# Kernel tuning notes

Hardware: AMD Instinct MI355X
Metric: run time of the kernel (lower is better)

Reference implementation:

```python
import jax, jax.numpy as jnp
import numpy as np

B, S, HS = 2, 2048, 2048
H, KVH, D = 8, 1, 256
ROPE_BASE = 10000.0


def _rope_cos_sin(position_ids, dim, base=ROPE_BASE):
    # position_ids: (B, S) int -> cos/sin: (B, S, dim)
    inv_freq = 1.0 / (base ** (jnp.arange(0, dim, 2, dtype=jnp.float32) / dim))
    thetas = position_ids.astype(jnp.float32)[..., None] * inv_freq  # (B,S,dim/2)
    emb = jnp.concatenate([thetas, thetas], axis=-1)  # (B,S,dim)
    return jnp.cos(emb), jnp.sin(emb)


def _rotate_half(x):
    x1, x2 = jnp.split(x, 2, axis=-1)
    return jnp.concatenate([-x2, x1], axis=-1)


def _apply_rope(q, k, cos, sin):
    # q,k: (B,h,S,D); cos,sin: (B,S,D) -> unsqueeze head dim
    cos = cos[:, None, :, :]
    sin = sin[:, None, :, :]
    q_emb = q * cos + _rotate_half(q) * sin
    k_emb = k * cos + _rotate_half(k) * sin
    return q_emb, k_emb


def setup_inputs() -> dict:
    key = jax.random.key(0)
    k0, k1, k2, k3, k4 = jax.random.split(key, 5)
    hidden_states = jax.random.normal(k0, (B, S, HS), jnp.float32)
    # causal additive mask: 0 where j<=i, large negative otherwise
    causal = jnp.tril(jnp.ones((S, S), dtype=bool))
    attention_mask = jnp.where(causal, 0.0, -1e9).astype(jnp.float32)
    attention_mask = jnp.broadcast_to(attention_mask[None, None], (B, 1, S, S))
    position_ids = jnp.broadcast_to(jnp.arange(S, dtype=jnp.int32)[None], (B, S))
    scale = 0.02
    Wq = jax.random.normal(k1, (HS, H * D), jnp.float32) * scale
    Wk = jax.random.normal(k2, (HS, KVH * D), jnp.float32) * scale
    Wv = jax.random.normal(k3, (HS, KVH * D), jnp.float32) * scale
    Wo = jax.random.normal(k4, (H * D, HS), jnp.float32) * scale
    return {"hidden_states": hidden_states, "attention_mask": attention_mask,
            "position_ids": position_ids, "Wq": Wq, "Wk": Wk, "Wv": Wv, "Wo": Wo}


def reference(hidden_states, attention_mask, position_ids, Wq, Wk, Wv, Wo):
    bs, seq_len, _ = hidden_states.shape
    q = (hidden_states @ Wq).reshape(bs, seq_len, H, D).transpose(0, 2, 1, 3)     # (B,H,S,D)
    k = (hidden_states @ Wk).reshape(bs, seq_len, KVH, D).transpose(0, 2, 1, 3)   # (B,KVH,S,D)
    v = (hidden_states @ Wv).reshape(bs, seq_len, KVH, D).transpose(0, 2, 1, 3)
    cos, sin = _rope_cos_sin(position_ids, D)
    q, k = _apply_rope(q, k, cos, sin)
    n_rep = H // KVH
    k = jnp.repeat(k, n_rep, axis=1)  # GQA repeat -> (B,H,S,D)
    v = jnp.repeat(v, n_rep, axis=1)
    scores = jnp.einsum('bhqd,bhkd->bhqk', q, k) / jnp.sqrt(jnp.float32(D))
    scores = scores + attention_mask
    attn = jax.nn.softmax(scores.astype(jnp.float32), axis=-1).astype(q.dtype)
    out = jnp.einsum('bhqk,bhkd->bhqd', attn, v)            # (B,H,S,D)
    out = out.transpose(0, 2, 1, 3).reshape(bs, seq_len, H * D)
    return out @ Wo
```

## Files before the change

kernel.cpp:

```cpp
#include <hip/hip_runtime.h>
#include <hip/hip_bf16.h>

typedef __bf16 bf16x8 __attribute__((ext_vector_type(8)));
typedef __bf16 bf16x4 __attribute__((ext_vector_type(4)));
typedef float  f32x4  __attribute__((ext_vector_type(4)));

#define MFMA16(a, b, c) __builtin_amdgcn_mfma_f32_16x16x32_bf16((a), (b), (c), 0, 0, 0)

#define GLOBAL_AS(p) ((const __attribute__((address_space(1))) void*)(p))
#define LDS_AS(p)    ((__attribute__((address_space(3))) void*)(p))

__global__ __launch_bounds__(256) void cvt_bf16_kernel(const float* __restrict__ in,
                                                       __bf16* __restrict__ out)
{
    const int idx = blockIdx.x * 256 + threadIdx.x;
    const float4* p = (const float4*)in + (size_t)idx * 2;
    float4 a = p[0], b = p[1];
    bf16x8 o;
    o[0] = (__bf16)a.x; o[1] = (__bf16)a.y; o[2] = (__bf16)a.z; o[3] = (__bf16)a.w;
    o[4] = (__bf16)b.x; o[5] = (__bf16)b.y; o[6] = (__bf16)b.z; o[7] = (__bf16)b.w;
    ((bf16x8*)out)[idx] = o;
}

__global__ __launch_bounds__(128) void trig_kernel(float2* __restrict__ cs)
{
    const int s = blockIdx.x, i = threadIdx.x;
    const float theta = (float)s * exp2f((float)i * (-13.287712379549449f / 128.f));
    float sn, c;
    sincosf(theta, &sn, &c);
    cs[s * 128 + i] = make_float2(c, sn);
}

__global__ __launch_bounds__(256) void transpose_cvt_kernel(const float* __restrict__ W,
                                                            __bf16* __restrict__ Bt,
                                                            int K, int N)
{
    __shared__ float t[32][33];
    const int n0 = blockIdx.x * 32, k0 = blockIdx.y * 32;
    const int x = threadIdx.x, y = threadIdx.y;
#pragma unroll
    for (int r = 0; r < 4; ++r)
        t[y + r * 8][x] = W[(size_t)(k0 + y + r * 8) * N + n0 + x];
    __syncthreads();
#pragma unroll
    for (int r = 0; r < 4; ++r)
        Bt[(size_t)(n0 + y + r * 8) * K + k0 + x] = (__bf16)t[x][y + r * 8];
}

__global__ __launch_bounds__(256) void vt_kernel(const __bf16* __restrict__ qkv,
                                                 __bf16* __restrict__ vT)
{
    __shared__ __bf16 t[32][33];
    const int s0 = blockIdx.x * 32, d0 = blockIdx.y * 32, b = blockIdx.z;
    const int x = threadIdx.x, y = threadIdx.y;
#pragma unroll
    for (int r = 0; r < 4; ++r)
        t[y + r * 8][x] = qkv[(size_t)(b * 2048 + s0 + y + r * 8) * 2560 + 2304 + d0 + x];
    __syncthreads();
#pragma unroll
    for (int r = 0; r < 4; ++r)
        vT[(size_t)(b * 256 + d0 + y + r * 8) * 2048 + s0 + x] = t[x][y + r * 8];
}

template <typename TC>
__global__ __launch_bounds__(256) void gemm_bt(const __bf16* __restrict__ A,
                                               const __bf16* __restrict__ Bt,
                                               TC* __restrict__ C,
                                               int M, int N, int K)
{
    __shared__ __bf16 As[128 * 32];
    __shared__ __bf16 Bs[128 * 32];

    const int tid  = threadIdx.x;
    const int wave = tid >> 6, lane = tid & 63;
    const int quad = lane >> 4, l16 = lane & 15;
    const int wm = (wave >> 1) * 64, wn = (wave & 1) * 64;
    const int bm = blockIdx.y * 128, bn = blockIdx.x * 128;

    f32x4 acc[4][4] = {};

    for (int k0 = 0; k0 < K; k0 += 32) {
        __syncthreads();
#pragma unroll
        for (int c = 0; c < 2; ++c) {
            const int off = tid * 16 + c * 4096;
            const int row = off >> 6;
            const int kb  = (off & 63) >> 1;
            const __bf16* ga = A  + (size_t)(bm + row) * K + k0 + kb;
            const __bf16* gb = Bt + (size_t)(bn + row) * K + k0 + kb;
            __builtin_amdgcn_global_load_lds(GLOBAL_AS(ga), LDS_AS(As + (off >> 1)), 16, 0, 0);
            __builtin_amdgcn_global_load_lds(GLOBAL_AS(gb), LDS_AS(Bs + (off >> 1)), 16, 0, 0);
        }
        __syncthreads();

        bf16x8 af[4];
#pragma unroll
        for (int mi = 0; mi < 4; ++mi)
            af[mi] = *(const bf16x8*)&As[(wm + mi * 16 + l16) * 32 + quad * 8];
#pragma unroll
        for (int ni = 0; ni < 4; ++ni) {
            bf16x8 bfr = *(const bf16x8*)&Bs[(wn + ni * 16 + l16) * 32 + quad * 8];
#pragma unroll
            for (int mi = 0; mi < 4; ++mi)
                acc[mi][ni] = MFMA16(af[mi], bfr, acc[mi][ni]);
        }
    }
#pragma unroll
    for (int mi = 0; mi < 4; ++mi)
#pragma unroll
        for (int ni = 0; ni < 4; ++ni)
#pragma unroll
            for (int r = 0; r < 4; ++r) {
                int row = bm + wm + mi * 16 + quad * 4 + r;
                int col = bn + wn + ni * 16 + l16;
                C[(size_t)row * N + col] = (TC)acc[mi][ni][r];
            }
}

__global__ __launch_bounds__(256) void rope_kernel(__bf16* __restrict__ qkv,
                                                   const float2* __restrict__ cs)
{
    const int bs = blockIdx.x;
    const int s = bs & 2047;
    const int t = threadIdx.x;
    const float QS = 0.09016843787599907f;

    const int hh = t >> 5, i0 = (t & 31) * 4;
    float2 c0 = cs[s * 128 + i0 + 0], c1 = cs[s * 128 + i0 + 1];
    float2 c2 = cs[s * 128 + i0 + 2], c3 = cs[s * 128 + i0 + 3];

    {
        __bf16* p = qkv + (size_t)bs * 2560 + hh * 256 + i0;
        bf16x4 x1 = *(const bf16x4*)p;
        bf16x4 x2 = *(const bf16x4*)(p + 128);
        bf16x4 o1, o2;
        o1[0] = (__bf16)(((float)x1[0] * c0.x - (float)x2[0] * c0.y) * QS);
        o2[0] = (__bf16)(((float)x2[0] * c0.x + (float)x1[0] * c0.y) * QS);
        o1[1] = (__bf16)(((float)x1[1] * c1.x - (float)x2[1] * c1.y) * QS);
        o2[1] = (__bf16)(((float)x2[1] * c1.x + (float)x1[1] * c1.y) * QS);
        o1[2] = (__bf16)(((float)x1[2] * c2.x - (float)x2[2] * c2.y) * QS);
        o2[2] = (__bf16)(((float)x2[2] * c2.x + (float)x1[2] * c2.y) * QS);
        o1[3] = (__bf16)(((float)x1[3] * c3.x - (float)x2[3] * c3.y) * QS);
        o2[3] = (__bf16)(((float)x2[3] * c3.x + (float)x1[3] * c3.y) * QS);
        *(bf16x4*)p = o1;
        *(bf16x4*)(p + 128) = o2;
    }
    if (t < 32) {
        const int j0 = t * 4;
        float2 d0 = cs[s * 128 + j0 + 0], d1 = cs[s * 128 + j0 + 1];
        float2 d2 = cs[s * 128 + j0 + 2], d3 = cs[s * 128 + j0 + 3];
        __bf16* p = qkv + (size_t)bs * 2560 + 2048 + j0;
        bf16x4 x1 = *(const bf16x4*)p;
        bf16x4 x2 = *(const bf16x4*)(p + 128);
        bf16x4 o1, o2;
        o1[0] = (__bf16)((float)x1[0] * d0.x - (float)x2[0] * d0.y);
        o2[0] = (__bf16)((float)x2[0] * d0.x + (float)x1[0] * d0.y);
        o1[1] = (__bf16)((float)x1[1] * d1.x - (float)x2[1] * d1.y);
        o2[1] = (__bf16)((float)x2[1] * d1.x + (float)x1[1] * d1.y);
        o1[2] = (__bf16)((float)x1[2] * d2.x - (float)x2[2] * d2.y);
        o2[2] = (__bf16)((float)x2[2] * d2.x + (float)x1[2] * d2.y);
        o1[3] = (__bf16)((float)x1[3] * d3.x - (float)x2[3] * d3.y);
        o2[3] = (__bf16)((float)x2[3] * d3.x + (float)x1[3] * d3.y);
        *(bf16x4*)p = o1;
        *(bf16x4*)(p + 128) = o2;
    }
}

static __device__ __forceinline__ void stage8(const __bf16* src, __bf16* dst,
                                              size_t src_step)
{
#pragma unroll
    for (int p = 0; p < 8; ++p)
        __builtin_amdgcn_global_load_lds(GLOBAL_AS(src + (size_t)p * src_step),
                                         LDS_AS(dst + p * 2048), 16, 0, 0);
}

__global__ __launch_bounds__(256, 2) void attn_kernel(const __bf16* __restrict__ qkv,
                                                      const __bf16* __restrict__ vTg,
                                                      __bf16* __restrict__ og)
{
    __shared__ __bf16 Ks[64 * 256];
    __shared__ __bf16 Vs[256 * 64];
    __shared__ __bf16 Ps[4][32][36];

    const int b = blockIdx.z, h = blockIdx.y;
    const int xx = (int)blockIdx.x;
    const int half = xx >> 1;
    const bool rev = ((xx & 1) == 0) ^ (b != 0);
    const int qt = rev ? 31 - half : half;
    const int q0 = qt * 64;
    const int tid  = threadIdx.x;
    const int wave = tid >> 6, lane = tid & 63;
    const int quad = lane >> 4, l16 = lane & 15;
    const int xork = l16 & 7;
    const int wm2 = wave >> 1, wn2 = wave & 1;

    bf16x8 onef;
#pragma unroll
    for (int e = 0; e < 8; ++e) onef[e] = (__bf16)1.0f;

    bf16x8 qf[2][8];
#pragma unroll
    for (int mi = 0; mi < 2; ++mi) {
        const __bf16* qptr = qkv + (size_t)(b * 2048 + q0 + wm2 * 32 + mi * 16 + l16) * 2560
                           + h * 256;
#pragma unroll
        for (int dc = 0; dc < 8; ++dc)
            qf[mi][dc] = *(const bf16x8*)(qptr + dc * 32 + quad * 8);
    }

    f32x4 oacc[2][16] = {};
    f32x4 lacc[2] = {};

    const int kKey0 = tid >> 5;
    const int kC    = (tid & 31) ^ (kKey0 & 7);
    const __bf16* kstage0 = qkv + (size_t)b * 2048 * 2560 + 2048
                          + (size_t)kKey0 * 2560 + kC * 8;
    const int vD0 = tid >> 3;
    const int vC  = (tid & 7) ^ (vD0 & 7);
    const __bf16* vstage0 = vTg + (size_t)b * 256 * 2048 + (size_t)vD0 * 2048 + vC * 8;
    __bf16* kdst = Ks + tid * 8;
    __bf16* vdst = Vs + tid * 8;

    int ckK[8];
#pragma unroll
    for (int dc = 0; dc < 8; ++dc) ckK[dc] = (dc * 4 + quad) ^ xork;
    const int chV = (wn2 * 4 + quad) ^ xork;

    stage8(kstage0, kdst, (size_t)8 * 2560);
    __builtin_amdgcn_sched_barrier(0);
    stage8(vstage0, vdst, (size_t)32 * 2048);
    __builtin_amdgcn_sched_barrier(0);

    for (int j0 = 0; j0 <= q0; j0 += 64) {
        const bool more = (j0 + 64 <= q0);

        asm volatile("s_waitcnt vmcnt(8)" ::: "memory");
        __builtin_amdgcn_s_barrier();
        __builtin_amdgcn_sched_barrier(0);

        f32x4 sc[2][2] = {};
        __builtin_amdgcn_s_setprio(1);
#pragma unroll
        for (int nt = 0; nt < 2; ++nt) {
            const __bf16* krow = &Ks[(wn2 * 32 + nt * 16 + l16) * 256];
#pragma unroll
            for (int dc = 0; dc < 8; ++dc) {
                bf16x8 kf = *(const bf16x8*)(krow + ckK[dc] * 8);
                sc[0][nt] = MFMA16(qf[0][dc], kf, sc[0][nt]);
                sc[1][nt] = MFMA16(qf[1][dc], kf, sc[1][nt]);
            }
        }
        __builtin_amdgcn_s_setprio(0);

        asm volatile("s_waitcnt lgkmcnt(0)" ::: "memory");
        __builtin_amdgcn_s_barrier();
        __builtin_amdgcn_sched_barrier(0);

        if (more) {
            stage8(kstage0 + (size_t)(j0 + 64) * 2560, kdst, (size_t)8 * 2560);
            __builtin_amdgcn_sched_barrier(0);
        }

        if (j0 == q0) {
#pragma unroll
            for (int nt = 0; nt < 2; ++nt) {
                int key = j0 + wn2 * 32 + nt * 16 + l16;
#pragma unroll
                for (int mi = 0; mi < 2; ++mi)
#pragma unroll
                    for (int r = 0; r < 4; ++r) {
                        int row = q0 + wm2 * 32 + mi * 16 + quad * 4 + r;
                        if (key > row) sc[mi][nt][r] = -1e30f;
                    }
            }
        }
#pragma unroll
        for (int mi = 0; mi < 2; ++mi)
#pragma unroll
            for (int nt = 0; nt < 2; ++nt)
#pragma unroll
                for (int r = 0; r < 4; ++r)
                    Ps[wave][mi * 16 + quad * 4 + r][nt * 16 + l16] =
                        (__bf16)exp2f(sc[mi][nt][r] - 8.f);
        bf16x8 pf0 = *(const bf16x8*)&Ps[wave][l16][quad * 8];
        bf16x8 pf1 = *(const bf16x8*)&Ps[wave][16 + l16][quad * 8];

        if (more) asm volatile("s_waitcnt vmcnt(8)" ::: "memory");
        else      asm volatile("s_waitcnt vmcnt(0)" ::: "memory");
        __builtin_amdgcn_s_barrier();
        __builtin_amdgcn_sched_barrier(0);

        __builtin_amdgcn_s_setprio(1);
#pragma unroll
        for (int dt = 0; dt < 16; ++dt) {
            const __bf16* vrow = &Vs[(dt * 16 + l16) * 64];
            bf16x8 vf = *(const bf16x8*)(vrow + chV * 8);
            oacc[0][dt] = MFMA16(pf0, vf, oacc[0][dt]);
            oacc[1][dt] = MFMA16(pf1, vf, oacc[1][dt]);
        }
        lacc[0] = MFMA16(pf0, onef, lacc[0]);
        lacc[1] = MFMA16(pf1, onef, lacc[1]);
        __builtin_amdgcn_s_setprio(0);

        asm volatile("s_waitcnt lgkmcnt(0)" ::: "memory");
        __builtin_amdgcn_s_barrier();
        __builtin_amdgcn_sched_barrier(0);

        if (more) {
            stage8(vstage0 + (j0 + 64), vdst, (size_t)32 * 2048);
            __builtin_amdgcn_sched_barrier(0);
        }
    }

    __syncthreads();
    float* oscr = (wm2 == 0) ? (float*)Ks : (float*)Vs;
    float* lscr = (float*)Ps;
    if (wn2 == 1) {
#pragma unroll
        for (int mi = 0; mi < 2; ++mi) {
#pragma unroll
            for (int dt = 0; dt < 16; ++dt)
#pragma unroll
                for (int r = 0; r < 4; ++r)
                    oscr[(mi * 16 + quad * 4 + r) * 256 + dt * 16 + l16] = oacc[mi][dt][r];
#pragma unroll
            for (int r = 0; r < 4; ++r)
                lscr[(wm2 * 32 + mi * 16 + quad * 4 + r) * 16 + l16] = lacc[mi][r];
        }
    }
    __syncthreads();
    if (wn2 == 0) {
#pragma unroll
        for (int mi = 0; mi < 2; ++mi) {
            float invl[4];
#pragma unroll
            for (int r = 0; r < 4; ++r)
                invl[r] = 1.f / (lacc[mi][r]
                        + lscr[(wm2 * 32 + mi * 16 + quad * 4 + r) * 16 + l16]);
#pragma unroll
            for (int dt = 0; dt < 16; ++dt)
#pragma unroll
                for (int r = 0; r < 4; ++r) {
                    float o = oacc[mi][dt][r]
                            + oscr[(mi * 16 + quad * 4 + r) * 256 + dt * 16 + l16];
                    int row = q0 + wm2 * 32 + mi * 16 + quad * 4 + r;
                    int col = h * 256 + dt * 16 + l16;
                    og[(size_t)(b * 2048 + row) * 2048 + col] = (__bf16)(o * invl[r]);
                }
        }
    }
}

extern "C" void kernel_launch(void* const* d_in, const int* in_sizes, int n_in,
                              void* d_out, int out_size, void* d_ws, size_t ws_size,
                              hipStream_t stream)
{
    (void)in_sizes; (void)n_in; (void)out_size; (void)ws_size;
    const float* hidden = (const float*)d_in[0];
    const float* Wq = (const float*)d_in[3];
    const float* Wk = (const float*)d_in[4];
    const float* Wv = (const float*)d_in[5];
    const float* Wo = (const float*)d_in[6];

    char* ws = (char*)d_ws;
    __bf16* hb    = (__bf16*)(ws);
    __bf16* qkv   = (__bf16*)(ws + (16u << 20));
    __bf16* vTb   = (__bf16*)(ws + (36u << 20));
    __bf16* ob    = (__bf16*)(ws + (38u << 20));
    __bf16* Wqkvt = (__bf16*)(ws + (54u << 20));
    __bf16* Wot   = (__bf16*)(ws + (64u << 20));
    float2* csb   = (float2*)(ws + (72u << 20));
    float* out = (float*)d_out;

    dim3 blk(256);
    dim3 tblk(32, 8);
    cvt_bf16_kernel<<<dim3(4096), blk, 0, stream>>>(hidden, hb);
    trig_kernel<<<dim3(2048), dim3(128), 0, stream>>>(csb);
    transpose_cvt_kernel<<<dim3(64, 64), tblk, 0, stream>>>(Wq, Wqkvt, 2048, 2048);
    transpose_cvt_kernel<<<dim3(8, 64), tblk, 0, stream>>>(Wk, Wqkvt + (size_t)2048 * 2048, 2048, 256);
    transpose_cvt_kernel<<<dim3(8, 64), tblk, 0, stream>>>(Wv, Wqkvt + (size_t)2304 * 2048, 2048, 256);
    transpose_cvt_kernel<<<dim3(64, 64), tblk, 0, stream>>>(Wo, Wot, 2048, 2048);
    gemm_bt<__bf16><<<dim3(20, 32), blk, 0, stream>>>(hb, Wqkvt, qkv, 4096, 2560, 2048);
    rope_kernel<<<dim3(4096), blk, 0, stream>>>(qkv, csb);
    vt_kernel<<<dim3(64, 8, 2), tblk, 0, stream>>>(qkv, vTb);
    attn_kernel<<<dim3(32, 8, 2), blk, 0, stream>>>(qkv, vTb, ob);
    gemm_bt<float><<<dim3(16, 32), blk, 0, stream>>>(ob, Wot, out, 4096, 2048, 2048);
}
```

Measured before the change: 355.8 us.

## Replace GEMM with triple-buffered, XOR-swizzled 512-thread pipelined kernel

```diff
diff --git a/kernel.cpp b/kernel.cpp
--- a/kernel.cpp
+++ b/kernel.cpp
@@ -63,48 +63,131 @@
 }
 
 template <typename TC>
-__global__ __launch_bounds__(256) void gemm_bt(const __bf16* __restrict__ A,
-                                               const __bf16* __restrict__ Bt,
-                                               TC* __restrict__ C,
-                                               int M, int N, int K)
-{
-    __shared__ __bf16 As[128 * 32];
-    __shared__ __bf16 Bs[128 * 32];
+__global__ __launch_bounds__(512, 2) void gemm_mp(const __bf16* __restrict__ A,
+                                                  const __bf16* __restrict__ Bt,
+                                                  TC* __restrict__ C,
+                                                  int M, int N, int K)
+{
+    __shared__ __bf16 As[3][128 * 64];
+    __shared__ __bf16 Bs[3][256 * 64];
 
     const int tid  = threadIdx.x;
     const int wave = tid >> 6, lane = tid & 63;
     const int quad = lane >> 4, l16 = lane & 15;
-    const int wm = (wave >> 1) * 64, wn = (wave & 1) * 64;
-    const int bm = blockIdx.y * 128, bn = blockIdx.x * 128;
+    const int wm = (wave >> 2) * 64, wn = (wave & 3) * 64;
+    const int bm = blockIdx.y * 128, bn = blockIdx.x * 256;
+    const int xk = l16 & 7;
+
+    const int srow = tid >> 3;
+    const int schk = (tid & 7) ^ (srow & 7);
+    const __bf16* gA[2];
+    const __bf16* gB[4];
+#pragma unroll
+    for (int p = 0; p < 2; ++p)
+        gA[p] = A + (size_t)(bm + p * 64 + srow) * K + schk * 8;
+#pragma unroll
+    for (int p = 0; p < 4; ++p)
+        gB[p] = Bt + (size_t)(bn + p * 64 + srow) * K + schk * 8;
+
+#define STAGE_A2(s, t) do {                                                       \
+    const size_t ko_ = (size_t)(t) * 64;                                          \
+    __builtin_amdgcn_global_load_lds(GLOBAL_AS(gA[0] + ko_),                      \
+        LDS_AS((char*)As[s] + tid * 16), 16, 0, 0);                               \
+    __builtin_amdgcn_global_load_lds(GLOBAL_AS(gA[1] + ko_),                      \
+        LDS_AS((char*)As[s] + 8192 + tid * 16), 16, 0, 0);                        \
+} while (0)
+#define STAGE_B01(s, t) do {                                                      \
+    const size_t ko_ = (size_t)(t) * 64;                                          \
+    __builtin_amdgcn_global_load_lds(GLOBAL_AS(gB[0] + ko_),                      \
+        LDS_AS((char*)Bs[s] + tid * 16), 16, 0, 0);                               \
+    __builtin_amdgcn_global_load_lds(GLOBAL_AS(gB[1] + ko_),                      \
+        LDS_AS((char*)Bs[s] + 8192 + tid * 16), 16, 0, 0);                        \
+} while (0)
+#define STAGE_B23(s, t) do {                                                      \
+    const size_t ko_ = (size_t)(t) * 64;                                          \
+    __builtin_amdgcn_global_load_lds(GLOBAL_AS(gB[2] + ko_),                      \
+        LDS_AS((char*)Bs[s] + 16384 + tid * 16), 16, 0, 0);                       \
+    __builtin_amdgcn_global_load_lds(GLOBAL_AS(gB[3] + ko_),                      \
+        LDS_AS((char*)Bs[s] + 24576 + tid * 16), 16, 0, 0);                       \
+} while (0)
 
     f32x4 acc[4][4] = {};
-
-    for (int k0 = 0; k0 < K; k0 += 32) {
-        __syncthreads();
-#pragma unroll
-        for (int c = 0; c < 2; ++c) {
-            const int off = tid * 16 + c * 4096;
-            const int row = off >> 6;
-            const int kb  = (off & 63) >> 1;
-            const __bf16* ga = A  + (size_t)(bm + row) * K + k0 + kb;
-            const __bf16* gb = Bt + (size_t)(bn + row) * K + k0 + kb;
-            __builtin_amdgcn_global_load_lds(GLOBAL_AS(ga), LDS_AS(As + (off >> 1)), 16, 0, 0);
-            __builtin_amdgcn_global_load_lds(GLOBAL_AS(gb), LDS_AS(Bs + (off >> 1)), 16, 0, 0);
-        }
-        __syncthreads();
-
-        bf16x8 af[4];
+    const int nk = K >> 6;
+
+    STAGE_A2(0, 0); STAGE_B01(0, 0); STAGE_B23(0, 0);
+    STAGE_A2(1, 1); STAGE_B01(1, 1); STAGE_B23(1, 1);
+    asm volatile("s_waitcnt vmcnt(6)" ::: "memory");
+    __builtin_amdgcn_s_barrier();
+
+    int s = 0;
+    for (int t = 0; t < nk; ++t) {
+        const int sp = (s + 2 >= 3) ? s - 1 : s + 2;
+        const bool more2 = (t + 2 < nk);
+        const bool more1 = (t + 1 < nk);
+
+        bf16x8 af[4][2], bfr[2][2];
 #pragma unroll
         for (int mi = 0; mi < 4; ++mi)
-            af[mi] = *(const bf16x8*)&As[(wm + mi * 16 + l16) * 32 + quad * 8];
-#pragma unroll
-        for (int ni = 0; ni < 4; ++ni) {
-            bf16x8 bfr = *(const bf16x8*)&Bs[(wn + ni * 16 + l16) * 32 + quad * 8];
-#pragma unroll
-            for (int mi = 0; mi < 4; ++mi)
-                acc[mi][ni] = MFMA16(af[mi], bfr, acc[mi][ni]);
-        }
-    }
+#pragma unroll
+            for (int kh = 0; kh < 2; ++kh)
+                af[mi][kh] = *(const bf16x8*)
+                    &As[s][(wm + mi * 16 + l16) * 64 + (((kh << 2) | quad) ^ xk) * 8];
+#pragma unroll
+        for (int ni = 0; ni < 2; ++ni)
+#pragma unroll
+            for (int kh = 0; kh < 2; ++kh)
+                bfr[ni][kh] = *(const bf16x8*)
+                    &Bs[s][(wn + ni * 16 + l16) * 64 + (((kh << 2) | quad) ^ xk) * 8];
+        if (more2) { STAGE_A2(sp, t + 2); STAGE_B01(sp, t + 2); }
+        __builtin_amdgcn_sched_barrier(0);
+        __builtin_amdgcn_s_barrier();
+        asm volatile("s_waitcnt lgkmcnt(0)" ::: "memory");
+        __builtin_amdgcn_sched_barrier(0);
+        __builtin_amdgcn_s_setprio(1);
+#pragma unroll
+        for (int ni = 0; ni < 2; ++ni)
+#pragma unroll
+            for (int mi = 0; mi < 4; ++mi) {
+                acc[mi][ni] = MFMA16(af[mi][0], bfr[ni][0], acc[mi][ni]);
+                acc[mi][ni] = MFMA16(af[mi][1], bfr[ni][1], acc[mi][ni]);
+            }
+        __builtin_amdgcn_s_setprio(0);
+        __builtin_amdgcn_sched_barrier(0);
+        __builtin_amdgcn_s_barrier();
+
+        bf16x8 bf2[2][2];
+#pragma unroll
+        for (int ni = 0; ni < 2; ++ni)
+#pragma unroll
+            for (int kh = 0; kh < 2; ++kh)
+                bf2[ni][kh] = *(const bf16x8*)
+                    &Bs[s][(wn + (2 + ni) * 16 + l16) * 64 + (((kh << 2) | quad) ^ xk) * 8];
+        if (more2) STAGE_B23(sp, t + 2);
+        __builtin_amdgcn_sched_barrier(0);
+        __builtin_amdgcn_s_barrier();
+        asm volatile("s_waitcnt lgkmcnt(0)" ::: "memory");
+        __builtin_amdgcn_sched_barrier(0);
+        __builtin_amdgcn_s_setprio(1);
+#pragma unroll
+        for (int ni = 0; ni < 2; ++ni)
+#pragma unroll
+            for (int mi = 0; mi < 4; ++mi) {
+                acc[mi][2 + ni] = MFMA16(af[mi][0], bf2[ni][0], acc[mi][2 + ni]);
+                acc[mi][2 + ni] = MFMA16(af[mi][1], bf2[ni][1], acc[mi][2 + ni]);
+            }
+        __builtin_amdgcn_s_setprio(0);
+        if (more1) {
+            if (more2) asm volatile("s_waitcnt vmcnt(6)" ::: "memory");
+            else       asm volatile("s_waitcnt vmcnt(0)" ::: "memory");
+        }
+        __builtin_amdgcn_sched_barrier(0);
+        __builtin_amdgcn_s_barrier();
+        s = (s + 1 == 3) ? 0 : s + 1;
+    }
+#undef STAGE_A2
+#undef STAGE_B01
+#undef STAGE_B23
+
 #pragma unroll
     for (int mi = 0; mi < 4; ++mi)
 #pragma unroll
@@ -374,6 +457,7 @@
     float* out = (float*)d_out;
 
     dim3 blk(256);
+    dim3 mpblk(512);
     dim3 tblk(32, 8);
     cvt_bf16_kernel<<<dim3(4096), blk, 0, stream>>>(hidden, hb);
     trig_kernel<<<dim3(2048), dim3(128), 0, stream>>>(csb);
@@ -381,9 +465,9 @@
     transpose_cvt_kernel<<<dim3(8, 64), tblk, 0, stream>>>(Wk, Wqkvt + (size_t)2048 * 2048, 2048, 256);
     transpose_cvt_kernel<<<dim3(8, 64), tblk, 0, stream>>>(Wv, Wqkvt + (size_t)2304 * 2048, 2048, 256);
     transpose_cvt_kernel<<<dim3(64, 64), tblk, 0, stream>>>(Wo, Wot, 2048, 2048);
-    gemm_bt<__bf16><<<dim3(20, 32), blk, 0, stream>>>(hb, Wqkvt, qkv, 4096, 2560, 2048);
+    gemm_mp<__bf16><<<dim3(10, 32), mpblk, 0, stream>>>(hb, Wqkvt, qkv, 4096, 2560, 2048);
     rope_kernel<<<dim3(4096), blk, 0, stream>>>(qkv, csb);
     vt_kernel<<<dim3(64, 8, 2), tblk, 0, stream>>>(qkv, vTb);
     attn_kernel<<<dim3(32, 8, 2), blk, 0, stream>>>(qkv, vTb, ob);
-    gemm_bt<float><<<dim3(16, 32), blk, 0, stream>>>(ob, Wot, out, 4096, 2048, 2048);
-}
+    gemm_mp<float><<<dim3(8, 32), mpblk, 0, stream>>>(ob, Wot, out, 4096, 2048, 2048);
+}
```

Measured after the change: 356.3 us. No clear change (+0.1%).
